# Kernel tuning notes

Hardware: AMD Instinct MI355X
Metric: run time of the kernel (lower is better)

Reference implementation:

```python
import jax, jax.numpy as jnp
import numpy as np

N_NODES = 100000


def _gcn_conv(x, W, b, src, dst, n):
    # PyG GCNConv: h = x @ W; add self-loops; norm = d^-1/2[src] * d^-1/2[dst];
    # out[i] = sum_{(s->i)} norm * h[s] + b
    h = x @ W  # [N, F_out]
    deg = jax.ops.segment_sum(jnp.ones_like(dst, dtype=h.dtype), dst, num_segments=n)
    dis = jnp.where(deg > 0, jax.lax.rsqrt(jnp.maximum(deg, 1.0)), 0.0)
    norm = dis[src] * dis[dst]  # [E]
    msg = h[src] * norm[:, None]  # [E, F_out] gather + scale
    out = jax.ops.segment_sum(msg, dst, num_segments=n)  # scatter-add
    return out + b


def _add_self_loops(edge_index, n):
    loops = jnp.arange(n, dtype=edge_index.dtype)
    src = jnp.concatenate([edge_index[0], loops])
    dst = jnp.concatenate([edge_index[1], loops])
    return src, dst


def setup_inputs() -> dict:
    key = jax.random.key(0)
    k_x, k_e, k_w1, k_w2 = jax.random.split(key, 4)
    n, e, f_in, f_hid = N_NODES, 1600000, 128, 64
    x = jax.random.normal(k_x, (n, f_in), dtype=jnp.float32)
    edge_index = jax.random.randint(k_e, (2, e), 0, n, dtype=jnp.int64)
    # Glorot-ish init for weights
    W1 = jax.random.normal(k_w1, (f_in, f_hid), dtype=jnp.float32) / np.sqrt(f_in)
    b1 = jnp.zeros((f_hid,), dtype=jnp.float32)
    W2 = jax.random.normal(k_w2, (f_hid, f_hid), dtype=jnp.float32) / np.sqrt(f_hid)
    b2 = jnp.zeros((f_hid,), dtype=jnp.float32)
    return {"x": x, "edge_index": edge_index, "W1": W1, "b1": b1, "W2": W2, "b2": b2}


def reference(x, edge_index, W1, b1, W2, b2):
    n = x.shape[0]
    src, dst = _add_self_loops(edge_index, n)
    h = jax.nn.relu(_gcn_conv(x, W1, b1, src, dst, n))
    # F.dropout(training=False) in eval mode is identity
    out = _gcn_conv(h, W2, b2, src, dst, n)
    return out
```

## Files before the change

### kernel.cpp

```cpp
#include <hip/hip_runtime.h>
#include <hip/hip_bf16.h>


#define FOUT 64
#define BW 256
#define BSH 8
#define MAXB 512
#define CHUNK 4096
#define SLAB 6144

__device__ __forceinline__ float bf2f(unsigned int u16) {
    union { unsigned int i; float f; } c;
    c.i = u16 << 16;
    return c.f;
}
__device__ __forceinline__ unsigned short f2bf(float f) {
    union { float f; unsigned int i; } c;
    c.f = f;
    unsigned int i = c.i;
    return (unsigned short)((i + 0x7FFFu + ((i >> 16) & 1u)) >> 16);
}

__global__ __launch_bounds__(512) void edge_hist(const int* __restrict__ dst,
                                                 int* __restrict__ cnt, int E) {
    __shared__ int h[MAXB];
    const int blk = blockIdx.x, t = threadIdx.x;
    h[t] = 0;
    __syncthreads();
    const int e0 = blk * CHUNK;
#pragma unroll
    for (int k = 0; k < CHUNK / 512; k++) {
        int e = e0 + k * 512 + t;
        if (e < E) atomicAdd(&h[dst[e] >> BSH], 1);
    }
    __syncthreads();
    cnt[blk * MAXB + t] = h[t];
}

__global__ __launch_bounds__(512) void col_scan(int* __restrict__ cnt, int nblk,
                                                int* __restrict__ gcnt) {
    __shared__ int ts[512];
    const int b = blockIdx.x;
    const int t = threadIdx.x;
    int v = (t < nblk) ? cnt[t * MAXB + b] : 0;
    ts[t] = v;
    __syncthreads();
    for (int off = 1; off < 512; off <<= 1) {
        int x = (t >= off) ? ts[t - off] : 0;
        __syncthreads();
        ts[t] += x;
        __syncthreads();
    }
    if (t < nblk) cnt[t * MAXB + b] = b * SLAB + ts[t] - v;
    if (t == 511) gcnt[b] = ts[511];
}

__global__ __launch_bounds__(512) void edge_place(
    const int* __restrict__ src, const int* __restrict__ dst,
    const int* __restrict__ cnt, int* __restrict__ ebuf, int E) {
    __shared__ int lbase[MAXB];
    __shared__ int cur[MAXB];
    const int blk = blockIdx.x, t = threadIdx.x;
    lbase[t] = cnt[blk * MAXB + t];
    cur[t] = 0;
    __syncthreads();
    const int e0 = blk * CHUNK;
#pragma unroll
    for (int k = 0; k < CHUNK / 512; k++) {
        int e = e0 + k * 512 + t;
        if (e < E) {
            int d = dst[e];
            int b = d >> BSH;
            int r = atomicAdd(&cur[b], 1);
            ebuf[lbase[b] + r] = src[e] | ((d & (BW - 1)) << 17);
        }
    }
}

__global__ __launch_bounds__(512) void csr_build(
    int* __restrict__ ebuf, const int* __restrict__ gcnt,
    unsigned int* __restrict__ rowinfo, float* __restrict__ dis, int n) {
    __shared__ int ldeg[BW];
    __shared__ int lscan[BW];
    const int b = blockIdx.x, t = threadIdx.x;
    const int node0 = b << BSH;
    const int nn = min(BW, n - node0);
    const int ebeg = b * SLAB;
    const int cnt = gcnt[b];

    int w[SLAB / 512];
#pragma unroll
    for (int k = 0; k < SLAB / 512; k++) {
        int idx = t + k * 512;
        w[k] = (idx < cnt) ? ebuf[ebeg + idx] : -1;
    }
    if (t < BW) ldeg[t] = 0;
    __syncthreads();
#pragma unroll
    for (int k = 0; k < SLAB / 512; k++)
        if (w[k] >= 0) atomicAdd(&ldeg[w[k] >> 17], 1);
    __syncthreads();
    int v = 0;
    if (t < BW) {
        v = ldeg[t];
        lscan[t] = v;
    }
    __syncthreads();
    for (int off = 1; off < BW; off <<= 1) {
        int x = 0;
        if (t < BW && t >= off) x = lscan[t - off];
        __syncthreads();
        if (t < BW) lscan[t] += x;
        __syncthreads();
    }
    if (t < nn) {
        int ex = lscan[t] - v;
        rowinfo[node0 + t] = ((unsigned int)(ebeg + ex) << 8) | (unsigned int)v;
        dis[node0 + t] = rsqrtf((float)v + 1.0f);
    }
    __syncthreads();
    if (t < BW) ldeg[t] = lscan[t] - v;
    __syncthreads();
#pragma unroll
    for (int k = 0; k < SLAB / 512; k++)
        if (w[k] >= 0) {
            int r = atomicAdd(&ldeg[w[k] >> 17], 1);
            ebuf[ebeg + r] = w[k] & 0x1FFFF;
        }
}

template <int K>
__global__ __launch_bounds__(256) void gemm_xw(const float* __restrict__ X,
                                               const float* __restrict__ W,
                                               const float* __restrict__ dis,
                                               unsigned short* __restrict__ HS, int n) {
    constexpr int KT = 32;
    constexpr int KP = KT + 4;
    __shared__ float xs[64 * KP];
    __shared__ float ws[KT * 64];
    const int tid  = threadIdx.x;
    const int row0 = blockIdx.x * 64;

    const int tr = tid >> 4;
    const int tc = tid & 15;
    float acc[4][4];
#pragma unroll
    for (int i = 0; i < 4; i++)
#pragma unroll
        for (int j = 0; j < 4; j++) acc[i][j] = 0.f;

    const int sxr = tid >> 3;
    const int sxc = (tid & 7) << 2;
    const int swk = tid >> 4;
    const int swc = (tid & 15) << 2;

#pragma unroll 1
    for (int k0 = 0; k0 < K; k0 += KT) {
#pragma unroll
        for (int l = 0; l < 2; l++) {
            int r = sxr + l * 32;
            float4 v = make_float4(0.f, 0.f, 0.f, 0.f);
            if (row0 + r < n) v = *(const float4*)&X[(size_t)(row0 + r) * K + k0 + sxc];
            *(float4*)&xs[r * KP + sxc] = v;
        }
#pragma unroll
        for (int l = 0; l < 2; l++) {
            int kk = swk + l * 16;
            *(float4*)&ws[kk * 64 + swc] = *(const float4*)&W[(size_t)(k0 + kk) * 64 + swc];
        }
        __syncthreads();
#pragma unroll
        for (int k = 0; k < KT; k += 4) {
            float4 xv[4], wv[4];
#pragma unroll
            for (int i = 0; i < 4; i++) xv[i] = *(float4*)&xs[(tr * 4 + i) * KP + k];
#pragma unroll
            for (int kk = 0; kk < 4; kk++) wv[kk] = *(float4*)&ws[(k + kk) * 64 + tc * 4];
#pragma unroll
            for (int i = 0; i < 4; i++) {
                float xi[4] = {xv[i].x, xv[i].y, xv[i].z, xv[i].w};
#pragma unroll
                for (int kk = 0; kk < 4; kk++) {
                    acc[i][0] = fmaf(xi[kk], wv[kk].x, acc[i][0]);
                    acc[i][1] = fmaf(xi[kk], wv[kk].y, acc[i][1]);
                    acc[i][2] = fmaf(xi[kk], wv[kk].z, acc[i][2]);
                    acc[i][3] = fmaf(xi[kk], wv[kk].w, acc[i][3]);
                }
            }
        }
        __syncthreads();
    }

#pragma unroll
    for (int i = 0; i < 4; i++) {
        int r = row0 + tr * 4 + i;
        if (r < n) {
            float dr = dis[r];
            ushort4 o;
            o.x = f2bf(acc[i][0] * dr);
            o.y = f2bf(acc[i][1] * dr);
            o.z = f2bf(acc[i][2] * dr);
            o.w = f2bf(acc[i][3] * dr);
            *(ushort4*)&HS[(size_t)r * FOUT + tc * 4] = o;
        }
    }
}

template <bool RELU>
__global__ __launch_bounds__(256) void aggregate(
    const unsigned int* __restrict__ hs32, const unsigned int* __restrict__ rowinfo,
    const int* __restrict__ col, const float* __restrict__ dis,
    const float* __restrict__ bias, float* __restrict__ out, int n) {
    const int wave = blockIdx.x * 4 + (threadIdx.x >> 6);
    const int lane = threadIdx.x & 63;
    const int half = lane >> 5;
    const int jj   = lane & 31;
    const int i = wave * 2 + half;
    if (i >= n) return;

    const unsigned int info = rowinfo[i];
    const int beg = (int)(info >> 8);
    const int end = beg + (int)(info & 255u);
    unsigned int su = hs32[(size_t)i * 32 + jj];
    float a0 = bf2f(su & 0xFFFFu);
    float a1 = bf2f(su >> 16);

    const int hb = half << 5;
    for (int chunk = beg; chunk < end; chunk += 32) {
        int m = end - chunk;
        if (m > 32) m = 32;
        int c = (jj < m) ? col[chunk + jj] : 0;
        int q = 0;
        for (; q + 4 <= m; q += 4) {
            int s0 = __shfl(c, hb + q);
            int s1 = __shfl(c, hb + q + 1);
            int s2 = __shfl(c, hb + q + 2);
            int s3 = __shfl(c, hb + q + 3);
            unsigned int u0 = hs32[(size_t)s0 * 32 + jj];
            unsigned int u1 = hs32[(size_t)s1 * 32 + jj];
            unsigned int u2 = hs32[(size_t)s2 * 32 + jj];
            unsigned int u3 = hs32[(size_t)s3 * 32 + jj];
            a0 += bf2f(u0 & 0xFFFFu) + bf2f(u1 & 0xFFFFu) +
                  bf2f(u2 & 0xFFFFu) + bf2f(u3 & 0xFFFFu);
            a1 += bf2f(u0 >> 16) + bf2f(u1 >> 16) +
                  bf2f(u2 >> 16) + bf2f(u3 >> 16);
        }
        for (; q < m; q++) {
            int s = __shfl(c, hb + q);
            unsigned int u = hs32[(size_t)s * 32 + jj];
            a0 += bf2f(u & 0xFFFFu);
            a1 += bf2f(u >> 16);
        }
    }
    float d = dis[i];
    float2 bb = ((const float2*)bias)[jj];
    float v0 = d * a0 + bb.x;
    float v1 = d * a1 + bb.y;
    if (RELU) {
        v0 = fmaxf(v0, 0.0f);
        v1 = fmaxf(v1, 0.0f);
    }
    ((float2*)out)[(size_t)i * 32 + jj] = make_float2(v0, v1);
}

extern "C" void kernel_launch(void* const* d_in, const int* in_sizes, int n_in,
                              void* d_out, int out_size, void* d_ws, size_t ws_size,
                              hipStream_t stream) {
    const float* x  = (const float*)d_in[0];
    const int*   ei = (const int*)d_in[1];
    const float* W1 = (const float*)d_in[2];
    const float* b1 = (const float*)d_in[3];
    const float* W2 = (const float*)d_in[4];
    const float* b2 = (const float*)d_in[5];

    const int n = in_sizes[0] / 128;
    const int E = in_sizes[1] / 2;
    const int* srcp = ei;
    const int* dstp = ei + E;

    float* out = (float*)d_out;

    const int B = (n + BW - 1) / BW;
    const int nblk = (E + CHUNK - 1) / CHUNK;

    int*            cnt     = (int*)d_ws;
    int*            gcnt    = cnt + 512 * MAXB;
    unsigned int*   rowinfo = (unsigned int*)(gcnt + MAXB);
    float*          dis     = (float*)(rowinfo + n);
    int*            ebuf    = (int*)(dis + n);
    unsigned short* hs      = (unsigned short*)(ebuf + (size_t)B * SLAB);

    edge_hist<<<nblk, 512, 0, stream>>>(dstp, cnt, E);
    col_scan<<<B, 512, 0, stream>>>(cnt, nblk, gcnt);
    edge_place<<<nblk, 512, 0, stream>>>(srcp, dstp, cnt, ebuf, E);
    csr_build<<<B, 512, 0, stream>>>(ebuf, gcnt, rowinfo, dis, n);

    gemm_xw<128><<<(n + 63) / 64, 256, 0, stream>>>(x, W1, dis, hs, n);
    aggregate<true><<<(n + 7) / 8, 256, 0, stream>>>(
        (const unsigned int*)hs, rowinfo, ebuf, dis, b1, out, n);

    gemm_xw<64><<<(n + 63) / 64, 256, 0, stream>>>(out, W2, dis, hs, n);
    aggregate<false><<<(n + 7) / 8, 256, 0, stream>>>(
        (const unsigned int*)hs, rowinfo, ebuf, dis, b2, out, n);
}
```

Baseline: 245.3 us.

## Replace FP32 SIMT GEMM with split-bf16 MFMA using prepacked weight fragments

The dense X@W step now runs on bf16 MFMA instructions (16x16x32), not FP32 FMAs through shared memory. FP32 accuracy is approximated with a hi/lo bf16 split and three MFMAs per tile (hi*hi, lo*hi, hi*lo). Weights are converted into per-lane MFMA fragment layout once, by block 0 of the edge histogram kernel, and stored in workspace. The GEMM is small next to the gather/scatter aggregation, so the overall effect may be limited. Output stores are now scattered 2-byte writes rather than ushort4.

```diff
diff --git a/kernel.cpp b/kernel.cpp
--- a/kernel.cpp
+++ b/kernel.cpp
@@ -9,6 +9,9 @@
 #define CHUNK 4096
 #define SLAB 6144
 
+#define NT1 1024
+#define NT2 512
+
 __device__ __forceinline__ float bf2f(unsigned int u16) {
     union { unsigned int i; float f; } c;
     c.i = u16 << 16;
@@ -21,8 +24,32 @@
     return (unsigned short)((i + 0x7FFFu + ((i >> 16) & 1u)) >> 16);
 }
 
-__global__ __launch_bounds__(512) void edge_hist(const int* __restrict__ dst,
-                                                 int* __restrict__ cnt, int E) {
+typedef __attribute__((ext_vector_type(8))) short short8v;
+typedef __attribute__((ext_vector_type(4))) float f32x4;
+
+__device__ __forceinline__ void conv_w_frag(const float* __restrict__ W,
+                                            unsigned short* __restrict__ WhF,
+                                            unsigned short* __restrict__ WlF,
+                                            int task) {
+    const int lane = task & 63;
+    const int cf = (task >> 6) & 3;
+    const int s = task >> 8;
+    const int q = lane >> 4, m = lane & 15;
+#pragma unroll
+    for (int j = 0; j < 8; j++) {
+        int k = s * 32 + q * 8 + j;
+        float x = W[(size_t)k * 64 + cf * 16 + m];
+        unsigned short h = f2bf(x);
+        WhF[(size_t)task * 8 + j] = h;
+        WlF[(size_t)task * 8 + j] = f2bf(x - bf2f(h));
+    }
+}
+
+__global__ __launch_bounds__(512) void edge_hist(
+    const int* __restrict__ dst, int* __restrict__ cnt, int E,
+    const float* __restrict__ W1, const float* __restrict__ W2,
+    unsigned short* __restrict__ whf1, unsigned short* __restrict__ wlf1,
+    unsigned short* __restrict__ whf2, unsigned short* __restrict__ wlf2) {
     __shared__ int h[MAXB];
     const int blk = blockIdx.x, t = threadIdx.x;
     h[t] = 0;
@@ -32,6 +59,12 @@
     for (int k = 0; k < CHUNK / 512; k++) {
         int e = e0 + k * 512 + t;
         if (e < E) atomicAdd(&h[dst[e] >> BSH], 1);
+    }
+    if (blk == 0) {
+        for (int task = t; task < NT1 + NT2; task += 512) {
+            if (task < NT1) conv_w_frag(W1, whf1, wlf1, task);
+            else            conv_w_frag(W2, whf2, wlf2, task - NT1);
+        }
     }
     __syncthreads();
     cnt[blk * MAXB + t] = h[t];
@@ -130,78 +163,67 @@
 }
 
 template <int K>
-__global__ __launch_bounds__(256) void gemm_xw(const float* __restrict__ X,
-                                               const float* __restrict__ W,
-                                               const float* __restrict__ dis,
-                                               unsigned short* __restrict__ HS, int n) {
-    constexpr int KT = 32;
-    constexpr int KP = KT + 4;
-    __shared__ float xs[64 * KP];
-    __shared__ float ws[KT * 64];
-    const int tid  = threadIdx.x;
-    const int row0 = blockIdx.x * 64;
-
-    const int tr = tid >> 4;
-    const int tc = tid & 15;
-    float acc[4][4];
-#pragma unroll
-    for (int i = 0; i < 4; i++)
-#pragma unroll
-        for (int j = 0; j < 4; j++) acc[i][j] = 0.f;
-
-    const int sxr = tid >> 3;
-    const int sxc = (tid & 7) << 2;
-    const int swk = tid >> 4;
-    const int swc = (tid & 15) << 2;
-
-#pragma unroll 1
-    for (int k0 = 0; k0 < K; k0 += KT) {
-#pragma unroll
-        for (int l = 0; l < 2; l++) {
-            int r = sxr + l * 32;
-            float4 v = make_float4(0.f, 0.f, 0.f, 0.f);
-            if (row0 + r < n) v = *(const float4*)&X[(size_t)(row0 + r) * K + k0 + sxc];
-            *(float4*)&xs[r * KP + sxc] = v;
-        }
-#pragma unroll
-        for (int l = 0; l < 2; l++) {
-            int kk = swk + l * 16;
-            *(float4*)&ws[kk * 64 + swc] = *(const float4*)&W[(size_t)(k0 + kk) * 64 + swc];
-        }
-        __syncthreads();
-#pragma unroll
-        for (int k = 0; k < KT; k += 4) {
-            float4 xv[4], wv[4];
-#pragma unroll
-            for (int i = 0; i < 4; i++) xv[i] = *(float4*)&xs[(tr * 4 + i) * KP + k];
-#pragma unroll
-            for (int kk = 0; kk < 4; kk++) wv[kk] = *(float4*)&ws[(k + kk) * 64 + tc * 4];
-#pragma unroll
-            for (int i = 0; i < 4; i++) {
-                float xi[4] = {xv[i].x, xv[i].y, xv[i].z, xv[i].w};
-#pragma unroll
-                for (int kk = 0; kk < 4; kk++) {
-                    acc[i][0] = fmaf(xi[kk], wv[kk].x, acc[i][0]);
-                    acc[i][1] = fmaf(xi[kk], wv[kk].y, acc[i][1]);
-                    acc[i][2] = fmaf(xi[kk], wv[kk].z, acc[i][2]);
-                    acc[i][3] = fmaf(xi[kk], wv[kk].w, acc[i][3]);
-                }
+__global__ __launch_bounds__(256) void gemm_xw_mfma(
+    const float* __restrict__ X,
+    const unsigned short* __restrict__ WhF,
+    const unsigned short* __restrict__ WlF,
+    const float* __restrict__ dis,
+    unsigned short* __restrict__ HS, int n) {
+    const int lane = threadIdx.x & 63;
+    const int wv = threadIdx.x >> 6;
+    const int wrow0 = blockIdx.x * 64 + wv * 16;
+    const int m = lane & 15;
+    const int q = lane >> 4;
+
+    f32x4 acc[4];
+#pragma unroll
+    for (int cf = 0; cf < 4; cf++) acc[cf] = (f32x4)0.f;
+
+    const int arow = wrow0 + m;
+    const bool rok = (arow < n);
+    const float* xp = X + (size_t)arow * K + q * 8;
+
+#pragma unroll
+    for (int s = 0; s < K / 32; s++) {
+        float4 v0, v1;
+        if (rok) {
+            v0 = *(const float4*)(xp + s * 32);
+            v1 = *(const float4*)(xp + s * 32 + 4);
+        } else {
+            v0 = make_float4(0.f, 0.f, 0.f, 0.f);
+            v1 = v0;
+        }
+        const float xa[8] = {v0.x, v0.y, v0.z, v0.w, v1.x, v1.y, v1.z, v1.w};
+        union { unsigned int u[4]; short8v v; } Ah, Al;
+#pragma unroll
+        for (int p = 0; p < 4; p++) {
+            unsigned short h0 = f2bf(xa[2 * p]);
+            unsigned short h1 = f2bf(xa[2 * p + 1]);
+            Ah.u[p] = (unsigned int)h0 | ((unsigned int)h1 << 16);
+            unsigned short l0 = f2bf(xa[2 * p] - bf2f(h0));
+            unsigned short l1 = f2bf(xa[2 * p + 1] - bf2f(h1));
+            Al.u[p] = (unsigned int)l0 | ((unsigned int)l1 << 16);
+        }
+        const unsigned short* wh = WhF + ((size_t)(s * 4) * 64 + lane) * 8;
+        const unsigned short* wl = WlF + ((size_t)(s * 4) * 64 + lane) * 8;
+#pragma unroll
+        for (int cf = 0; cf < 4; cf++) {
+            short8v bh = *(const short8v*)(wh + (size_t)cf * 64 * 8);
+            short8v bl = *(const short8v*)(wl + (size_t)cf * 64 * 8);
+            acc[cf] = __builtin_amdgcn_mfma_f32_16x16x32_bf16(Ah.v, bh, acc[cf], 0, 0, 0);
+            acc[cf] = __builtin_amdgcn_mfma_f32_16x16x32_bf16(Al.v, bh, acc[cf], 0, 0, 0);
+            acc[cf] = __builtin_amdgcn_mfma_f32_16x16x32_bf16(Ah.v, bl, acc[cf], 0, 0, 0);
+        }
+    }
+#pragma unroll
+    for (int r = 0; r < 4; r++) {
+        int row = wrow0 + q * 4 + r;
+        if (row < n) {
+            float dr = dis[row];
+#pragma unroll
+            for (int cf = 0; cf < 4; cf++) {
+                HS[(size_t)row * FOUT + cf * 16 + m] = f2bf(acc[cf][r] * dr);
             }
-        }
-        __syncthreads();
-    }
-
-#pragma unroll
-    for (int i = 0; i < 4; i++) {
-        int r = row0 + tr * 4 + i;
-        if (r < n) {
-            float dr = dis[r];
-            ushort4 o;
-            o.x = f2bf(acc[i][0] * dr);
-            o.y = f2bf(acc[i][1] * dr);
-            o.z = f2bf(acc[i][2] * dr);
-            o.w = f2bf(acc[i][3] * dr);
-            *(ushort4*)&HS[(size_t)r * FOUT + tc * 4] = o;
         }
     }
 }
@@ -289,17 +311,22 @@
     float*          dis     = (float*)(rowinfo + n);
     int*            ebuf    = (int*)(dis + n);
     unsigned short* hs      = (unsigned short*)(ebuf + (size_t)B * SLAB);
-
-    edge_hist<<<nblk, 512, 0, stream>>>(dstp, cnt, E);
+    unsigned short* whf1    = hs + (size_t)n * FOUT;
+    unsigned short* wlf1    = whf1 + (size_t)NT1 * 8;
+    unsigned short* whf2    = wlf1 + (size_t)NT1 * 8;
+    unsigned short* wlf2    = whf2 + (size_t)NT2 * 8;
+
+    edge_hist<<<nblk, 512, 0, stream>>>(dstp, cnt, E, W1, W2,
+                                        whf1, wlf1, whf2, wlf2);
     col_scan<<<B, 512, 0, stream>>>(cnt, nblk, gcnt);
     edge_place<<<nblk, 512, 0, stream>>>(srcp, dstp, cnt, ebuf, E);
     csr_build<<<B, 512, 0, stream>>>(ebuf, gcnt, rowinfo, dis, n);
 
-    gemm_xw<128><<<(n + 63) / 64, 256, 0, stream>>>(x, W1, dis, hs, n);
+    gemm_xw_mfma<128><<<(n + 63) / 64, 256, 0, stream>>>(x, whf1, wlf1, dis, hs, n);
     aggregate<true><<<(n + 7) / 8, 256, 0, stream>>>(
         (const unsigned int*)hs, rowinfo, ebuf, dis, b1, out, n);
 
-    gemm_xw<64><<<(n + 63) / 64, 256, 0, stream>>>(out, W2, dis, hs, n);
+    gemm_xw_mfma<64><<<(n + 63) / 64, 256, 0, stream>>>(out, whf2, wlf2, dis, hs, n);
     aggregate<false><<<(n + 7) / 8, 256, 0, stream>>>(
         (const unsigned int*)hs, rowinfo, ebuf, dis, b2, out, n);
 }
```

Result: faster. 231.9 us (-5.5%).
